# Kernel optimization log

Hardware: AMD Instinct MI355X
Metric: run time of the kernel (lower is better)

The kernel has to match this reference:

```python
import jax, jax.numpy as jnp
import numpy as np

N_HEADS = 8
D_EMBED = 512
D_HEAD = D_EMBED // N_HEADS
BS, SEQ = 2, 4096


def setup_inputs() -> dict:
    key = jax.random.key(0)
    ks = jax.random.split(key, 9)
    s = 1.0 / np.sqrt(D_EMBED)
    inp = {
        "x": jax.random.normal(ks[0], (BS, SEQ, D_EMBED), dtype=jnp.float32),
        "wq": jax.random.uniform(ks[1], (D_EMBED, D_EMBED), jnp.float32, -s, s),
        "bq": jax.random.uniform(ks[2], (D_EMBED,), jnp.float32, -s, s),
        "wk": jax.random.uniform(ks[3], (D_EMBED, D_EMBED), jnp.float32, -s, s),
        "bk": jax.random.uniform(ks[4], (D_EMBED,), jnp.float32, -s, s),
        "wv": jax.random.uniform(ks[5], (D_EMBED, D_EMBED), jnp.float32, -s, s),
        "bv": jax.random.uniform(ks[6], (D_EMBED,), jnp.float32, -s, s),
        "wo": jax.random.uniform(ks[7], (D_EMBED, D_EMBED), jnp.float32, -s, s),
        "bo": jax.random.uniform(ks[8], (D_EMBED,), jnp.float32, -s, s),
        "causal_mask": 1,
    }
    return inp


def reference(x, wq, bq, wk, bk, wv, bv, wo, bo, causal_mask):
    bs, seq, d = x.shape
    # torch Linear: y = x @ W^T + b, then SiLU gate
    q = jax.nn.silu(jnp.einsum('bsd,ed->bse', x, wq) + bq)
    k = jax.nn.silu(jnp.einsum('bsd,ed->bse', x, wk) + bk)
    v = jax.nn.silu(jnp.einsum('bsd,ed->bse', x, wv) + bv)
    # split heads: [b, h, s, dh]
    q = q.reshape(bs, seq, N_HEADS, D_HEAD).transpose(0, 2, 1, 3)
    k = k.reshape(bs, seq, N_HEADS, D_HEAD).transpose(0, 2, 1, 3)
    v = v.reshape(bs, seq, N_HEADS, D_HEAD).transpose(0, 2, 1, 3)
    scores = jnp.einsum('bhqd,bhkd->bhqk', q, k)  # [b,h,s,s]
    if causal_mask:
        mask = jnp.triu(jnp.ones((seq, seq), dtype=bool), k=1)
        scores = jnp.where(mask, -jnp.inf, scores)
    scores = scores / jnp.sqrt(jnp.asarray(D_HEAD, dtype=scores.dtype))
    attn = jax.nn.softmax(scores, axis=-1)
    out = jnp.einsum('bhqk,bhkd->bhqd', attn, v)
    out = out.transpose(0, 2, 1, 3).reshape(bs, seq, d)
    return jnp.einsum('bsd,ed->bse', out, wo) + bo
```

## Files before the change

### kernel.cpp

```cpp
#include <hip/hip_runtime.h>
#include <stdint.h>


typedef float  f32x4  __attribute__((ext_vector_type(4)));
typedef float  f32x16 __attribute__((ext_vector_type(16)));
typedef short  bf16x8 __attribute__((ext_vector_type(8)));
typedef unsigned int u32x4 __attribute__((ext_vector_type(4)));

#define DEV static __device__ __forceinline__

#define BSZ   2
#define SEQL  4096
#define NHEAD 8
#define DHEAD 64
#define DEMB  512
#define MROWS (BSZ*SEQL)
#define NXE   (MROWS*DEMB)
#define NWE   (DEMB*DEMB)

DEV void async_copy16(const void* g, void* l) {
  __builtin_amdgcn_global_load_lds(
      (const __attribute__((address_space(1))) void*)g,
      (__attribute__((address_space(3))) void*)l,
      16, 0, 0);
}

DEV unsigned short f2bf_bits(float f) {
  unsigned int x = __float_as_uint(f);
  x = x + 0x7FFFu + ((x >> 16) & 1u);
  return (unsigned short)(x >> 16);
}

__global__ __launch_bounds__(256) void convert_all(
    const float* __restrict__ x,
    const float* __restrict__ wq, const float* __restrict__ wk,
    const float* __restrict__ wv, const float* __restrict__ wo,
    unsigned short* __restrict__ dst)
{
  const int nch = (NXE + 4 * NWE) / 4;
  for (int c = blockIdx.x * 256 + threadIdx.x; c < nch; c += gridDim.x * 256) {
    const int off = c * 4;
    const float* src;
    int rel;
    if (off < NXE) {
      src = x; rel = off;
    } else {
      int rr = off - NXE;
      int j = rr >> 18;
      rel = rr & (NWE - 1);
      src = (j == 0) ? wq : (j == 1) ? wk : (j == 2) ? wv : wo;
    }
    float4 v = *(const float4*)(src + rel);
    ushort4 o = make_ushort4(f2bf_bits(v.x), f2bf_bits(v.y),
                             f2bf_bits(v.z), f2bf_bits(v.w));
    *(ushort4*)(dst + off) = o;
  }
}

DEV void gemm_mainloop(const unsigned short* __restrict__ A,
                       const unsigned short* __restrict__ B,
                       int arow0, int brow0,
                       unsigned short* Ash, unsigned short* Bsh,
                       int t, f32x4 acc[4][4])
{
  const int l = t & 63;
  const int w = t >> 6, wr = w >> 1, wc = w & 1;
  for (int kt = 0; kt < 8; ++kt) {
    const int k0 = kt * 64;
#pragma unroll
    for (int i = 0; i < 4; ++i) {
      int p = t + i * 256;
      int r = p >> 3;
      int c0 = ((p & 7) ^ (r & 7)) * 8;
      async_copy16(A + (size_t)(arow0 + r) * DEMB + k0 + c0, (char*)Ash + p * 16);
      async_copy16(B + (size_t)(brow0 + r) * DEMB + k0 + c0, (char*)Bsh + p * 16);
    }
    __syncthreads();

    bf16x8 af[4][2], bf[4][2];
#pragma unroll
    for (int m = 0; m < 4; ++m)
#pragma unroll
      for (int ks = 0; ks < 2; ++ks) {
        int r = wr * 64 + m * 16 + (l & 15);
        int c = (ks * 4 + (l >> 4)) ^ (r & 7);
        af[m][ks] = *(const bf16x8*)((const char*)Ash + r * 128 + c * 16);
      }
#pragma unroll
    for (int n = 0; n < 4; ++n)
#pragma unroll
      for (int ks = 0; ks < 2; ++ks) {
        int r = wc * 64 + n * 16 + (l & 15);
        int c = (ks * 4 + (l >> 4)) ^ (r & 7);
        bf[n][ks] = *(const bf16x8*)((const char*)Bsh + r * 128 + c * 16);
      }
#pragma unroll
    for (int m = 0; m < 4; ++m)
#pragma unroll
      for (int n = 0; n < 4; ++n)
#pragma unroll
        for (int ks = 0; ks < 2; ++ks)
          acc[m][n] = __builtin_amdgcn_mfma_f32_16x16x32_bf16(
              af[m][ks], bf[n][ks], acc[m][n], 0, 0, 0);
    __syncthreads();
  }
}

__global__ __launch_bounds__(256) void qkv_gemm(
    const unsigned short* __restrict__ xb,
    const unsigned short* __restrict__ wqb,
    const unsigned short* __restrict__ wkb,
    const unsigned short* __restrict__ wvb,
    const float* __restrict__ bq, const float* __restrict__ bk,
    const float* __restrict__ bv,
    unsigned short* __restrict__ q_out,
    unsigned short* __restrict__ k_out,
    unsigned short* __restrict__ v_out)
{
  __shared__ unsigned short Ash[128 * 64];
  __shared__ unsigned short Bsh[128 * 64];
  const int z = blockIdx.z;
  const unsigned short* W = (z == 0) ? wqb : (z == 1) ? wkb : wvb;
  const float* bias = (z == 0) ? bq : (z == 1) ? bk : bv;
  unsigned short* dst = (z == 0) ? q_out : (z == 1) ? k_out : v_out;

  f32x4 acc[4][4];
#pragma unroll
  for (int m = 0; m < 4; ++m)
#pragma unroll
    for (int n = 0; n < 4; ++n) acc[m][n] = (f32x4){0.f, 0.f, 0.f, 0.f};

  gemm_mainloop(xb, W, blockIdx.x * 128, blockIdx.y * 128, Ash, Bsh,
                threadIdx.x, acc);

  const int t = threadIdx.x, l = t & 63, w = t >> 6, wr = w >> 1, wc = w & 1;
  const float qscale = (z == 0) ? 0.18033688011112042f : 1.0f;
#pragma unroll
  for (int n = 0; n < 4; ++n) {
    const int e = blockIdx.y * 128 + wc * 64 + n * 16 + (l & 15);
    const float bval = bias[e];
    const int h = e >> 6, d = e & 63;
#pragma unroll
    for (int m = 0; m < 4; ++m)
#pragma unroll
      for (int g = 0; g < 4; ++g) {
        const int R = blockIdx.x * 128 + wr * 64 + m * 16 + (l >> 4) * 4 + g;
        float v = acc[m][n][g] + bval;
        v = v / (1.0f + __expf(-v));
        v *= qscale;
        const int b = R >> 12, s = R & 4095;
        const int head = b * NHEAD + h;
        size_t off;
        if (z == 1) {
          const int kt = s >> 5, ql = s & 31;
          const int dt = d >> 4, hi = (d >> 3) & 1, ee = d & 7;
          const int lane = (hi << 5) | ql;
          off = (size_t)head * (SEQL * DHEAD) +
                (size_t)(((kt << 2) + dt) << 9) + (lane << 3) + ee;
        } else if (z == 2) {
          const int kt = s >> 5, hf = (s >> 4) & 1, hi = (s >> 3) & 1, ee = s & 7;
          const int nn = d >> 5, ql = d & 31;
          const int lane = (hi << 5) | ql;
          off = (size_t)head * (SEQL * DHEAD) +
                (size_t)((((kt << 1) + nn) << 1) + hf) * 512 + (lane << 3) + ee;
        } else {
          off = (((size_t)head) * SEQL + s) * DHEAD + d;
        }
        dst[off] = f2bf_bits(v);
      }
  }
}

__global__ __launch_bounds__(256) void attn_fwd(
    const unsigned short* __restrict__ qb,
    const unsigned short* __restrict__ kfb,
    const unsigned short* __restrict__ vfb,
    unsigned short* __restrict__ attnb,
    const int* __restrict__ causal_ptr)
{
  __shared__ float Osh[2][32][65];
  __shared__ float Lsh[2][32];

  const int t = threadIdx.x;
  const int l = t & 63;
  const int ql = l & 31;
  const int hi = l >> 5;
  const int wid = t >> 6;
  const int r = wid & 1;
  const int h = wid >> 1;
  const int bid = blockIdx.x;
  const int cc = bid & 255, qq = bid >> 8;
  const int g = cc >> 4;
  const int head = cc & 15;
  const int j = (qq == 0) ? (63 - g) : (qq == 1) ? g
              : (qq == 2) ? (47 - g) : (16 + g);
  const int q0w = j * 64 + r * 32;
  const int causal = causal_ptr[0];

  const unsigned short* qbase = qb + (size_t)head * SEQL * DHEAD;
  const unsigned short* kbase = kfb + (size_t)head * SEQL * DHEAD;
  const unsigned short* vbase = vfb + (size_t)head * SEQL * DHEAD;

  bf16x8 qf[4];
#pragma unroll
  for (int dt = 0; dt < 4; ++dt)
    qf[dt] = *(const bf16x8*)(qbase +
        (unsigned)((q0w + ql) * DHEAD + dt * 16 + hi * 8));

  f32x16 o0, o1;
#pragma unroll
  for (int i = 0; i < 16; ++i) { o0[i] = 0.f; o1[i] = 0.f; }
  float rl = 0.f;

  const int T = causal ? 2 * (j + 1) : (SEQL / 32);
  const int ktm = (T + 1) >> 1;
  const int kt0 = h ? ktm : 0;
  const int kt1 = h ? T : ktm;

  const unsigned l8 = (unsigned)(l << 3);

  for (int kt = kt0; kt < kt1; ++kt) {
    const int k0 = kt * 32;

    const unsigned short* kp = kbase + ((unsigned)(kt << 2) << 9) + l8;
    bf16x8 kf[4];
#pragma unroll
    for (int dt = 0; dt < 4; ++dt)
      kf[dt] = *(const bf16x8*)(kp + (dt << 9));

    const unsigned short* vp = vbase + ((unsigned)(kt << 2) << 9) + l8;
    bf16x8 vf[2][2];
#pragma unroll
    for (int n = 0; n < 2; ++n)
#pragma unroll
      for (int hf = 0; hf < 2; ++hf)
        vf[n][hf] = *(const bf16x8*)(vp + (((n << 1) + hf) << 9));

    f32x16 s;
#pragma unroll
    for (int i = 0; i < 16; ++i) s[i] = 0.f;
#pragma unroll
    for (int dt = 0; dt < 4; ++dt)
      s = __builtin_amdgcn_mfma_f32_32x32x16_bf16(kf[dt], qf[dt], s, 0, 0, 0);

    if (causal && (k0 + 31 > q0w)) {
      const int qrow = q0w + ql;
#pragma unroll
      for (int rg = 0; rg < 16; ++rg) {
        const int kk = k0 + (rg & 3) + 8 * (rg >> 2) + 4 * hi;
        s[rg] = (kk > qrow) ? -1e30f : s[rg];
      }
    }

#pragma unroll
    for (int rg = 0; rg < 16; ++rg)
      s[rg] = __builtin_amdgcn_exp2f(s[rg]);

    rl += (((s[0] + s[1]) + (s[2] + s[3])) + ((s[4] + s[5]) + (s[6] + s[7])))
        + (((s[8] + s[9]) + (s[10] + s[11])) + ((s[12] + s[13]) + (s[14] + s[15])));

#pragma unroll
    for (int hf = 0; hf < 2; ++hf) {
      const int b8 = hf * 8;
      float e0 = s[b8 + 0], e1 = s[b8 + 1], e2 = s[b8 + 2], e3 = s[b8 + 3];
      float e4 = s[b8 + 4], e5 = s[b8 + 5], e6 = s[b8 + 6], e7 = s[b8 + 7];
      unsigned a0, a1, b0, b1;
      asm("v_cvt_pk_bf16_f32 %0, %1, %2" : "=v"(a0) : "v"(e0), "v"(e1));
      asm("v_cvt_pk_bf16_f32 %0, %1, %2" : "=v"(a1) : "v"(e2), "v"(e3));
      asm("v_cvt_pk_bf16_f32 %0, %1, %2" : "=v"(b0) : "v"(e4), "v"(e5));
      asm("v_cvt_pk_bf16_f32 %0, %1, %2" : "=v"(b1) : "v"(e6), "v"(e7));
      asm("v_permlane32_swap_b32 %0, %1" : "+v"(a0), "+v"(b0));
      asm("v_permlane32_swap_b32 %0, %1" : "+v"(a1), "+v"(b1));
      u32x4 pau = {a0, a1, b0, b1};
      bf16x8 pa = *(bf16x8*)&pau;
      o0 = __builtin_amdgcn_mfma_f32_32x32x16_bf16(pa, vf[0][hf], o0, 0, 0, 0);
      o1 = __builtin_amdgcn_mfma_f32_32x32x16_bf16(pa, vf[1][hf], o1, 0, 0, 0);
    }
  }

  rl += __shfl_xor(rl, 32);

  if (h == 1) {
#pragma unroll
    for (int rg = 0; rg < 16; ++rg) {
      const int cr = (rg & 3) + 8 * (rg >> 2) + 4 * hi;
      Osh[r][cr][ql] = o0[rg];
      Osh[r][cr][32 + ql] = o1[rg];
    }
    if (l < 32) Lsh[r][l] = rl;
  }
  __syncthreads();
  if (h == 0) {
    const float inv = 1.0f / (rl + Lsh[r][ql]);
    const int b2 = head >> 3, hh = head & 7;
#pragma unroll
    for (int rg = 0; rg < 16; ++rg) {
      const int cr = (rg & 3) + 8 * (rg >> 2) + 4 * hi;
      const float invr = __shfl(inv, cr);
      const int srow = q0w + cr;
      const float v0 = (o0[rg] + Osh[r][cr][ql]) * invr;
      const float v1 = (o1[rg] + Osh[r][cr][32 + ql]) * invr;
      unsigned short* dst = attnb + ((size_t)b2 * SEQL + srow) * DEMB + hh * DHEAD;
      dst[ql] = f2bf_bits(v0);
      dst[32 + ql] = f2bf_bits(v1);
    }
  }
}

__global__ __launch_bounds__(256) void out_gemm(
    const unsigned short* __restrict__ ab,
    const unsigned short* __restrict__ wob,
    const float* __restrict__ bo,
    float* __restrict__ out)
{
  __shared__ unsigned short Ash[128 * 64];
  __shared__ unsigned short Bsh[128 * 64];
  f32x4 acc[4][4];
#pragma unroll
  for (int m = 0; m < 4; ++m)
#pragma unroll
    for (int n = 0; n < 4; ++n) acc[m][n] = (f32x4){0.f, 0.f, 0.f, 0.f};

  gemm_mainloop(ab, wob, blockIdx.x * 128, blockIdx.y * 128, Ash, Bsh,
                threadIdx.x, acc);

  const int t = threadIdx.x, l = t & 63, w = t >> 6, wr = w >> 1, wc = w & 1;
#pragma unroll
  for (int n = 0; n < 4; ++n) {
    const int e = blockIdx.y * 128 + wc * 64 + n * 16 + (l & 15);
    const float bval = bo[e];
#pragma unroll
    for (int m = 0; m < 4; ++m)
#pragma unroll
      for (int g = 0; g < 4; ++g) {
        const int R = blockIdx.x * 128 + wr * 64 + m * 16 + (l >> 4) * 4 + g;
        out[(size_t)R * DEMB + e] = acc[m][n][g] + bval;
      }
  }
}

extern "C" void kernel_launch(void* const* d_in, const int* in_sizes, int n_in,
                              void* d_out, int out_size, void* d_ws, size_t ws_size,
                              hipStream_t stream)
{
  const float* x  = (const float*)d_in[0];
  const float* wq = (const float*)d_in[1];
  const float* bq = (const float*)d_in[2];
  const float* wk = (const float*)d_in[3];
  const float* bk = (const float*)d_in[4];
  const float* wv = (const float*)d_in[5];
  const float* bv = (const float*)d_in[6];
  const float* wo = (const float*)d_in[7];
  const float* bo = (const float*)d_in[8];
  const int* causal = (const int*)d_in[9];
  float* out = (float*)d_out;

  unsigned short* ws  = (unsigned short*)d_ws;
  unsigned short* xb  = ws;
  unsigned short* wqb = xb + NXE;
  unsigned short* wkb = wqb + NWE;
  unsigned short* wvb = wkb + NWE;
  unsigned short* wob = wvb + NWE;
  unsigned short* qb  = wob + NWE;
  unsigned short* kfb = qb + NXE;
  unsigned short* vfb = kfb + NXE;
  unsigned short* atb = vfb + NXE;

  convert_all<<<dim3(1024), dim3(256), 0, stream>>>(x, wq, wk, wv, wo, xb);
  qkv_gemm<<<dim3(64, 4, 3), dim3(256), 0, stream>>>(
      xb, wqb, wkb, wvb, bq, bk, bv, qb, kfb, vfb);
  attn_fwd<<<dim3(1024), dim3(256), 0, stream>>>(qb, kfb, vfb, atb, causal);
  out_gemm<<<dim3(64, 4, 1), dim3(256), 0, stream>>>(atb, wob, bo, out);
}
```

Before: 108.5 us.

## Split attention KV range across four waves per 32-row slab with paired causal tiles

```diff
diff --git a/kernel.cpp b/kernel.cpp
--- a/kernel.cpp
+++ b/kernel.cpp
@@ -171,35 +171,19 @@
   }
 }
 
-__global__ __launch_bounds__(256) void attn_fwd(
-    const unsigned short* __restrict__ qb,
-    const unsigned short* __restrict__ kfb,
-    const unsigned short* __restrict__ vfb,
-    unsigned short* __restrict__ attnb,
-    const int* __restrict__ causal_ptr)
-{
-  __shared__ float Osh[2][32][65];
-  __shared__ float Lsh[2][32];
-
-  const int t = threadIdx.x;
-  const int l = t & 63;
-  const int ql = l & 31;
-  const int hi = l >> 5;
-  const int wid = t >> 6;
-  const int r = wid & 1;
-  const int h = wid >> 1;
-  const int bid = blockIdx.x;
-  const int cc = bid & 255, qq = bid >> 8;
-  const int g = cc >> 4;
-  const int head = cc & 15;
-  const int j = (qq == 0) ? (63 - g) : (qq == 1) ? g
-              : (qq == 2) ? (47 - g) : (16 + g);
+DEV void process_slab(const unsigned short* __restrict__ qb,
+                      const unsigned short* __restrict__ kfb,
+                      const unsigned short* __restrict__ vfb,
+                      unsigned short* __restrict__ attnb,
+                      int head, int j, int r, int causal,
+                      int ql, int hi, int l, int e, int t,
+                      float (*Osh)[32][65], float (*Lsh)[32])
+{
   const int q0w = j * 64 + r * 32;
-  const int causal = causal_ptr[0];
-
   const unsigned short* qbase = qb + (size_t)head * SEQL * DHEAD;
   const unsigned short* kbase = kfb + (size_t)head * SEQL * DHEAD;
   const unsigned short* vbase = vfb + (size_t)head * SEQL * DHEAD;
+  const unsigned l8 = (unsigned)(l << 3);
 
   bf16x8 qf[4];
 #pragma unroll
@@ -212,12 +196,9 @@
   for (int i = 0; i < 16; ++i) { o0[i] = 0.f; o1[i] = 0.f; }
   float rl = 0.f;
 
-  const int T = causal ? 2 * (j + 1) : (SEQL / 32);
-  const int ktm = (T + 1) >> 1;
-  const int kt0 = h ? ktm : 0;
-  const int kt1 = h ? T : ktm;
-
-  const unsigned l8 = (unsigned)(l << 3);
+  const int T = causal ? (2 * j + r + 1) : (SEQL / 32);
+  const int kt0 = (T * e) >> 2;
+  const int kt1 = (T * (e + 1)) >> 2;
 
   for (int kt = kt0; kt < kt1; ++kt) {
     const int k0 = kt * 32;
@@ -280,31 +261,59 @@
 
   rl += __shfl_xor(rl, 32);
 
-  if (h == 1) {
-#pragma unroll
-    for (int rg = 0; rg < 16; ++rg) {
-      const int cr = (rg & 3) + 8 * (rg >> 2) + 4 * hi;
-      Osh[r][cr][ql] = o0[rg];
-      Osh[r][cr][32 + ql] = o1[rg];
-    }
-    if (l < 32) Lsh[r][l] = rl;
-  }
+#pragma unroll
+  for (int rg = 0; rg < 16; ++rg) {
+    const int cr = (rg & 3) + 8 * (rg >> 2) + 4 * hi;
+    Osh[e][cr][ql] = o0[rg];
+    Osh[e][cr][32 + ql] = o1[rg];
+  }
+  if (l < 32) Lsh[e][l] = rl;
   __syncthreads();
-  if (h == 0) {
-    const float inv = 1.0f / (rl + Lsh[r][ql]);
+
+  {
+    const int row = t >> 3;
+    const int c0 = (t & 7) * 8;
+    const float inv = 1.0f /
+        (Lsh[0][row] + Lsh[1][row] + Lsh[2][row] + Lsh[3][row]);
     const int b2 = head >> 3, hh = head & 7;
-#pragma unroll
-    for (int rg = 0; rg < 16; ++rg) {
-      const int cr = (rg & 3) + 8 * (rg >> 2) + 4 * hi;
-      const float invr = __shfl(inv, cr);
-      const int srow = q0w + cr;
-      const float v0 = (o0[rg] + Osh[r][cr][ql]) * invr;
-      const float v1 = (o1[rg] + Osh[r][cr][32 + ql]) * invr;
-      unsigned short* dst = attnb + ((size_t)b2 * SEQL + srow) * DEMB + hh * DHEAD;
-      dst[ql] = f2bf_bits(v0);
-      dst[32 + ql] = f2bf_bits(v1);
-    }
-  }
+    const int srow = q0w + row;
+    bf16x8 ov;
+#pragma unroll
+    for (int jj = 0; jj < 8; ++jj) {
+      const float v = (Osh[0][row][c0 + jj] + Osh[1][row][c0 + jj] +
+                       Osh[2][row][c0 + jj] + Osh[3][row][c0 + jj]) * inv;
+      ov[jj] = (short)f2bf_bits(v);
+    }
+    *(bf16x8*)(attnb + ((size_t)b2 * SEQL + srow) * DEMB + hh * DHEAD + c0) = ov;
+  }
+  __syncthreads();
+}
+
+__global__ __launch_bounds__(256) void attn_fwd(
+    const unsigned short* __restrict__ qb,
+    const unsigned short* __restrict__ kfb,
+    const unsigned short* __restrict__ vfb,
+    unsigned short* __restrict__ attnb,
+    const int* __restrict__ causal_ptr)
+{
+  __shared__ float Osh[4][32][65];
+  __shared__ float Lsh[4][32];
+
+  const int t = threadIdx.x;
+  const int l = t & 63;
+  const int ql = l & 31;
+  const int hi = l >> 5;
+  const int e = t >> 6;
+  const int bid = blockIdx.x;
+  const int head = bid & 15;
+  const int p = (bid >> 4) & 31;
+  const int r = bid >> 9;
+  const int causal = causal_ptr[0];
+
+  process_slab(qb, kfb, vfb, attnb, head, 63 - p, r, causal,
+               ql, hi, l, e, t, Osh, Lsh);
+  process_slab(qb, kfb, vfb, attnb, head, p, r, causal,
+               ql, hi, l, e, t, Osh, Lsh);
 }
 
 __global__ __launch_bounds__(256) void out_gemm(
```

New measurement: 112.5 us. +3.7%, slower.
